# Optimization experiments

Hardware: AMD Instinct MI355X
Metric: run time of the kernel (lower is better)

The kernel has to match this reference:

```python
import jax, jax.numpy as jnp
import numpy as np

B = 131072
_CNOT_PERM = np.array([0, 1, 3, 2])  # |c t>: 10<->11 swap


def _apply_1q(psi, mats, wire):
    # psi: [B,2,2,2,2] complex, mats: [B,2,2] complex, per-sample single-qubit gate on `wire`
    psi = jnp.moveaxis(psi, wire + 1, -1)
    sh = psi.shape
    psi = psi.reshape(sh[0], -1, 2)
    psi = jnp.einsum('bij,bkj->bki', mats, psi)
    return jnp.moveaxis(psi.reshape(sh), -1, wire + 1)


def _cnot_adj(psi, w):
    # CNOT with control=w, target=w+1 (adjacent wires)
    psi = jnp.moveaxis(psi, (w + 1, w + 2), (-2, -1))
    sh = psi.shape
    psi = psi.reshape(sh[:-2] + (4,))[..., _CNOT_PERM].reshape(sh)
    return jnp.moveaxis(psi, (-2, -1), (w + 1, w + 2))


def _circuit(enc):
    # enc: [B,4] rotation angles; returns [B,4] PauliZ expectations
    b = enc.shape[0]
    half = 0.5 * enc
    c = jnp.cos(half).astype(jnp.complex64)
    s = jnp.sin(half).astype(jnp.complex64)
    z = jnp.zeros_like(c)
    ph = jnp.exp(-1j * half.astype(jnp.complex64))
    ry = jnp.stack([jnp.stack([c, -s], -1), jnp.stack([s, c], -1)], -2)   # [B,4,2,2]
    rz = jnp.stack([jnp.stack([ph, z], -1), jnp.stack([z, jnp.conj(ph)], -1)], -2)
    rx = jnp.stack([jnp.stack([c, -1j * s], -1), jnp.stack([-1j * s, c], -1)], -2)
    psi = jnp.zeros((b, 2, 2, 2, 2), jnp.complex64).at[:, 0, 0, 0, 0].set(1.0)
    for w in range(4):
        psi = _apply_1q(psi, ry[:, w], w)
    for w in range(4):
        psi = _apply_1q(psi, rz[:, w], w)
    for w in range(3):
        psi = _cnot_adj(psi, w)
    for w in range(4):
        psi = _apply_1q(psi, rx[:, w], w)
    probs = psi.real ** 2 + psi.imag ** 2  # [B,2,2,2,2]
    expz = []
    for w in range(4):
        p = jnp.moveaxis(probs, w + 1, 1).reshape(b, 2, -1).sum(-1)
        expz.append(p[:, 0] - p[:, 1])
    return jnp.stack(expz, -1)  # [B,4]


def setup_inputs() -> dict:
    key = jax.random.key(0)
    ks = jax.random.split(key, 9)
    f32 = jnp.float32
    return {
        'x': jax.random.normal(ks[0], (B, 1, 24, 24), f32),
        'W_enc': jax.random.normal(ks[1], (4, 16), f32) * 0.25,
        'b_enc': jax.random.normal(ks[2], (4,), f32) * 0.25,
        'W1': jax.random.normal(ks[3], (32, 4), f32) * 0.5,
        'b1': jax.random.normal(ks[4], (32,), f32) * 0.5,
        'W2': jax.random.normal(ks[5], (4, 32), f32) * 0.17,
        'b2': jax.random.normal(ks[6], (4,), f32) * 0.17,
        'gamma': jnp.ones((4,), f32),
        'beta': jnp.zeros((4,), f32),
    }


def reference(x, W_enc, b_enc, W1, b1, W2, b2, gamma, beta):
    bsz = x.shape[0]
    # avg_pool2d(x, 6): 24x24 -> 4x4, then flatten to 16
    pooled = x.reshape(bsz, 1, 4, 6, 4, 6).mean((3, 5)).reshape(bsz, 16)
    encoded = pooled @ W_enc.T + b_enc            # [B,4]
    out_q = _circuit(encoded)                      # [B,4]
    h = jax.nn.relu(out_q @ W1.T + b1)             # [B,32]
    out = h @ W2.T + b2                            # [B,num_classes]
    # BatchNorm1d in training mode (biased batch variance, eps=1e-5)
    mean = out.mean(0)
    var = ((out - mean) ** 2).mean(0)
    return gamma * (out - mean) / jnp.sqrt(var + 1e-5) + beta
```

## Files before the change

### kernel.cpp

```cpp
#include <hip/hip_runtime.h>

#define BATCH   131072
#define NBLK    512

__global__ __launch_bounds__(256) void qnat_main(
    const float* __restrict__ x,
    const float* __restrict__ Wenc, const float* __restrict__ benc,
    const float* __restrict__ W1,   const float* __restrict__ b1,
    const float* __restrict__ W2,   const float* __restrict__ b2,
    float* __restrict__ out_pre, float* __restrict__ partials)
{
    __shared__ float sW[360];
    const int t = threadIdx.x;
    if (t < 64)  sW[t]       = Wenc[t];
    if (t < 4)   sW[64 + t]  = benc[t];
    if (t < 128) sW[68 + t]  = W1[t];
    if (t < 32)  sW[196 + t] = b1[t];
    if (t < 128) sW[228 + t] = W2[t];
    if (t < 4)   sW[356 + t] = b2[t];
    __syncthreads();

    const int s = blockIdx.x * 256 + t;
    const float4* xp = reinterpret_cast<const float4*>(x + (size_t)s * 576);

    float pooled[16];
    #pragma unroll
    for (int pr = 0; pr < 4; ++pr) {
        float a0 = 0.f, a1 = 0.f, a2 = 0.f, a3 = 0.f;
        #pragma unroll
        for (int rr = 0; rr < 6; ++rr) {
            const float4* row = xp + (pr * 6 + rr) * 6;
            float4 va = row[0], vb = row[1], vc = row[2];
            float4 vd = row[3], ve = row[4], vf = row[5];
            a0 += va.x + va.y + va.z + va.w + vb.x + vb.y;
            a1 += vb.z + vb.w + vc.x + vc.y + vc.z + vc.w;
            a2 += vd.x + vd.y + vd.z + vd.w + ve.x + ve.y;
            a3 += ve.z + ve.w + vf.x + vf.y + vf.z + vf.w;
        }
        pooled[pr * 4 + 0] = a0 * (1.f / 36.f);
        pooled[pr * 4 + 1] = a1 * (1.f / 36.f);
        pooled[pr * 4 + 2] = a2 * (1.f / 36.f);
        pooled[pr * 4 + 3] = a3 * (1.f / 36.f);
    }

    float ch[4], sh[4];
    #pragma unroll
    for (int j = 0; j < 4; ++j) {
        float e = sW[64 + j];
        #pragma unroll
        for (int k = 0; k < 16; ++k) e = fmaf(pooled[k], sW[j * 16 + k], e);
        const float h = 0.5f * e;
        ch[j] = cosf(h);
        sh[j] = sinf(h);
    }

    float re[16], im[16];
    #pragma unroll
    for (int i = 0; i < 16; ++i) { re[i] = 0.f; im[i] = 0.f; }
    re[0] = 1.f;

    #pragma unroll
    for (int w = 0; w < 4; ++w) {
        const int bit = 8 >> w;
        #pragma unroll
        for (int i = 0; i < 16; ++i) if (!(i & bit)) {
            const int j = i | bit;
            const float r0 = re[i], m0 = im[i], r1 = re[j], m1 = im[j];
            re[i] = ch[w] * r0 - sh[w] * r1;  im[i] = ch[w] * m0 - sh[w] * m1;
            re[j] = sh[w] * r0 + ch[w] * r1;  im[j] = sh[w] * m0 + ch[w] * m1;
        }
    }
    #pragma unroll
    for (int w = 0; w < 4; ++w) {
        const int bit = 8 >> w;
        #pragma unroll
        for (int i = 0; i < 16; ++i) {
            const float sg = (i & bit) ? 1.f : -1.f;
            const float r = re[i], m = im[i];
            re[i] = ch[w] * r - sg * sh[w] * m;
            im[i] = ch[w] * m + sg * sh[w] * r;
        }
    }
    #define SWAP_AMP(a, b) { float tr = re[a]; re[a] = re[b]; re[b] = tr; \
                             float ti = im[a]; im[a] = im[b]; im[b] = ti; }
    SWAP_AMP(8, 12)  SWAP_AMP(9, 13)  SWAP_AMP(10, 14) SWAP_AMP(11, 15)
    SWAP_AMP(4, 6)   SWAP_AMP(5, 7)   SWAP_AMP(12, 14) SWAP_AMP(13, 15)
    SWAP_AMP(2, 3)   SWAP_AMP(6, 7)   SWAP_AMP(10, 11) SWAP_AMP(14, 15)
    #undef SWAP_AMP

    #pragma unroll
    for (int w = 0; w < 4; ++w) {
        const int bit = 8 >> w;
        #pragma unroll
        for (int i = 0; i < 16; ++i) if (!(i & bit)) {
            const int j = i | bit;
            const float r0 = re[i], m0 = im[i], r1 = re[j], m1 = im[j];
            re[i] = ch[w] * r0 + sh[w] * m1;  im[i] = ch[w] * m0 - sh[w] * r1;
            re[j] = sh[w] * m0 + ch[w] * r1;  im[j] = ch[w] * m1 - sh[w] * r0;
        }
    }

    float ez[4];
    #pragma unroll
    for (int w = 0; w < 4; ++w) {
        const int bit = 8 >> w;
        float acc = 0.f;
        #pragma unroll
        for (int i = 0; i < 16; ++i) {
            const float p = re[i] * re[i] + im[i] * im[i];
            acc += (i & bit) ? -p : p;
        }
        ez[w] = acc;
    }

    float o0 = sW[356], o1 = sW[357], o2 = sW[358], o3 = sW[359];
    #pragma unroll
    for (int i = 0; i < 32; ++i) {
        float h = sW[196 + i];
        #pragma unroll
        for (int j = 0; j < 4; ++j) h = fmaf(ez[j], sW[68 + i * 4 + j], h);
        h = fmaxf(h, 0.f);
        o0 = fmaf(h, sW[228 +  0 + i], o0);
        o1 = fmaf(h, sW[228 + 32 + i], o1);
        o2 = fmaf(h, sW[228 + 64 + i], o2);
        o3 = fmaf(h, sW[228 + 96 + i], o3);
    }

    reinterpret_cast<float4*>(out_pre)[s] = make_float4(o0, o1, o2, o3);

    float v[8] = { o0, o1, o2, o3, o0 * o0, o1 * o1, o2 * o2, o3 * o3 };
    #pragma unroll
    for (int off = 32; off; off >>= 1) {
        #pragma unroll
        for (int k = 0; k < 8; ++k) v[k] += __shfl_down(v[k], off);
    }
    __shared__ float red[4][8];
    const int wave = t >> 6, lane = t & 63;
    if (lane == 0) {
        #pragma unroll
        for (int k = 0; k < 8; ++k) red[wave][k] = v[k];
    }
    __syncthreads();
    if (t < 8) {
        partials[blockIdx.x * 8 + t] = red[0][t] + red[1][t] + red[2][t] + red[3][t];
    }
}

__global__ __launch_bounds__(512) void qnat_reduce(
    const float* __restrict__ partials, const float* __restrict__ gamma,
    const float* __restrict__ beta, float* __restrict__ ss)
{
    const int t = threadIdx.x;
    const float4* p4 = reinterpret_cast<const float4*>(partials);
    const float4 a = p4[t * 2], b = p4[t * 2 + 1];
    float v[8] = { a.x, a.y, a.z, a.w, b.x, b.y, b.z, b.w };
    #pragma unroll
    for (int off = 32; off; off >>= 1) {
        #pragma unroll
        for (int k = 0; k < 8; ++k) v[k] += __shfl_down(v[k], off);
    }
    __shared__ float red[8][8];
    const int wave = t >> 6, lane = t & 63;
    if (lane == 0) {
        #pragma unroll
        for (int k = 0; k < 8; ++k) red[wave][k] = v[k];
    }
    __syncthreads();
    if (t < 4) {
        float sum = 0.f, sumsq = 0.f;
        #pragma unroll
        for (int w = 0; w < 8; ++w) { sum += red[w][t]; sumsq += red[w][4 + t]; }
        const float invB  = 1.f / (float)BATCH;
        const float mean  = sum * invB;
        const float var   = sumsq * invB - mean * mean;
        const float scale = gamma[t] / sqrtf(var + 1e-5f);
        ss[t]     = scale;
        ss[4 + t] = beta[t] - mean * scale;
    }
}

__global__ __launch_bounds__(256) void qnat_bn(
    float* __restrict__ io, const float* __restrict__ ss)
{
    __shared__ float s8[8];
    if (threadIdx.x < 8) s8[threadIdx.x] = ss[threadIdx.x];
    __syncthreads();
    const int idx = blockIdx.x * 256 + threadIdx.x;
    float4* p = reinterpret_cast<float4*>(io);
    float4 v = p[idx];
    v.x = fmaf(v.x, s8[0], s8[4]);
    v.y = fmaf(v.y, s8[1], s8[5]);
    v.z = fmaf(v.z, s8[2], s8[6]);
    v.w = fmaf(v.w, s8[3], s8[7]);
    p[idx] = v;
}

extern "C" void kernel_launch(void* const* d_in, const int* in_sizes, int n_in,
                              void* d_out, int out_size, void* d_ws, size_t ws_size,
                              hipStream_t stream)
{
    const float* x     = (const float*)d_in[0];
    const float* Wenc  = (const float*)d_in[1];
    const float* benc  = (const float*)d_in[2];
    const float* W1    = (const float*)d_in[3];
    const float* b1    = (const float*)d_in[4];
    const float* W2    = (const float*)d_in[5];
    const float* b2    = (const float*)d_in[6];
    const float* gamma = (const float*)d_in[7];
    const float* beta  = (const float*)d_in[8];

    float* out      = (float*)d_out;
    float* partials = (float*)d_ws;
    float* ss       = partials + NBLK * 8;

    qnat_main<<<NBLK, 256, 0, stream>>>(x, Wenc, benc, W1, b1, W2, b2, out, partials);
    qnat_reduce<<<1, 512, 0, stream>>>(partials, gamma, beta, ss);
    qnat_bn<<<NBLK, 256, 0, stream>>>(out, ss);
}
```

Measured before the change: 71.71 us.

## Fuse main, reduce and batchnorm kernels via cooperative grid sync

Merges the three kernels into one cooperative kernel. After each block writes its partial sums, a grid-wide sync lets every block reduce all partials redundantly and apply batchnorm directly to its in-register outputs. This removes two kernel launches and the write-then-reread of the pre-normalized output. In exchange it adds a grid barrier, redundant per-block reduction of 4096 partials, and depends on all 512 blocks being co-resident.

New measurement: 152.8 us. 2.13x slower.

```diff
diff --git a/kernel.cpp b/kernel.cpp
--- a/kernel.cpp
+++ b/kernel.cpp
@@ -1,16 +1,21 @@
 #include <hip/hip_runtime.h>
+#include <hip/hip_cooperative_groups.h>
+
+namespace cg = cooperative_groups;
 
 #define BATCH   131072
 #define NBLK    512
 
-__global__ __launch_bounds__(256) void qnat_main(
+__global__ __launch_bounds__(256, 2) void qnat_fused(
     const float* __restrict__ x,
     const float* __restrict__ Wenc, const float* __restrict__ benc,
     const float* __restrict__ W1,   const float* __restrict__ b1,
     const float* __restrict__ W2,   const float* __restrict__ b2,
-    float* __restrict__ out_pre, float* __restrict__ partials)
+    const float* __restrict__ gamma, const float* __restrict__ beta,
+    float* __restrict__ out, float* __restrict__ partials)
 {
     __shared__ float sW[360];
+    __shared__ float red[4][8];
     const int t = threadIdx.x;
     if (t < 64)  sW[t]       = Wenc[t];
     if (t < 4)   sW[64 + t]  = benc[t];
@@ -126,73 +131,61 @@
         o3 = fmaf(h, sW[228 + 96 + i], o3);
     }
 
-    reinterpret_cast<float4*>(out_pre)[s] = make_float4(o0, o1, o2, o3);
-
-    float v[8] = { o0, o1, o2, o3, o0 * o0, o1 * o1, o2 * o2, o3 * o3 };
-    #pragma unroll
-    for (int off = 32; off; off >>= 1) {
-        #pragma unroll
-        for (int k = 0; k < 8; ++k) v[k] += __shfl_down(v[k], off);
-    }
-    __shared__ float red[4][8];
-    const int wave = t >> 6, lane = t & 63;
-    if (lane == 0) {
-        #pragma unroll
-        for (int k = 0; k < 8; ++k) red[wave][k] = v[k];
-    }
-    __syncthreads();
-    if (t < 8) {
-        partials[blockIdx.x * 8 + t] = red[0][t] + red[1][t] + red[2][t] + red[3][t];
-    }
-}
-
-__global__ __launch_bounds__(512) void qnat_reduce(
-    const float* __restrict__ partials, const float* __restrict__ gamma,
-    const float* __restrict__ beta, float* __restrict__ ss)
-{
-    const int t = threadIdx.x;
-    const float4* p4 = reinterpret_cast<const float4*>(partials);
-    const float4 a = p4[t * 2], b = p4[t * 2 + 1];
-    float v[8] = { a.x, a.y, a.z, a.w, b.x, b.y, b.z, b.w };
-    #pragma unroll
-    for (int off = 32; off; off >>= 1) {
-        #pragma unroll
-        for (int k = 0; k < 8; ++k) v[k] += __shfl_down(v[k], off);
-    }
-    __shared__ float red[8][8];
-    const int wave = t >> 6, lane = t & 63;
-    if (lane == 0) {
-        #pragma unroll
-        for (int k = 0; k < 8; ++k) red[wave][k] = v[k];
-    }
-    __syncthreads();
-    if (t < 4) {
-        float sum = 0.f, sumsq = 0.f;
-        #pragma unroll
-        for (int w = 0; w < 8; ++w) { sum += red[w][t]; sumsq += red[w][4 + t]; }
+    {
+        float v[8] = { o0, o1, o2, o3, o0 * o0, o1 * o1, o2 * o2, o3 * o3 };
+        #pragma unroll
+        for (int off = 32; off; off >>= 1) {
+            #pragma unroll
+            for (int k = 0; k < 8; ++k) v[k] += __shfl_down(v[k], off);
+        }
+        const int wave = t >> 6, lane = t & 63;
+        if (lane == 0) {
+            #pragma unroll
+            for (int k = 0; k < 8; ++k) red[wave][k] = v[k];
+        }
+        __syncthreads();
+        if (t < 8) {
+            partials[blockIdx.x * 8 + t] = red[0][t] + red[1][t] + red[2][t] + red[3][t];
+        }
+    }
+
+    cg::this_grid().sync();
+
+    {
+        const float4* p4 = reinterpret_cast<const float4*>(partials);
+        const float4 a0 = p4[t * 4 + 0], a1 = p4[t * 4 + 1];
+        const float4 a2 = p4[t * 4 + 2], a3 = p4[t * 4 + 3];
+        float v[8] = { a0.x + a2.x, a0.y + a2.y, a0.z + a2.z, a0.w + a2.w,
+                       a1.x + a3.x, a1.y + a3.y, a1.z + a3.z, a1.w + a3.w };
+        #pragma unroll
+        for (int off = 32; off; off >>= 1) {
+            #pragma unroll
+            for (int k = 0; k < 8; ++k) v[k] += __shfl_down(v[k], off);
+        }
+        const int wave = t >> 6, lane = t & 63;
+        __syncthreads();
+        if (lane == 0) {
+            #pragma unroll
+            for (int k = 0; k < 8; ++k) red[wave][k] = v[k];
+        }
+        __syncthreads();
+    }
+
+    float sc[4], sf[4];
+    #pragma unroll
+    for (int j = 0; j < 4; ++j) {
+        const float sum   = red[0][j] + red[1][j] + red[2][j] + red[3][j];
+        const float sumsq = red[0][4 + j] + red[1][4 + j] + red[2][4 + j] + red[3][4 + j];
         const float invB  = 1.f / (float)BATCH;
         const float mean  = sum * invB;
         const float var   = sumsq * invB - mean * mean;
-        const float scale = gamma[t] / sqrtf(var + 1e-5f);
-        ss[t]     = scale;
-        ss[4 + t] = beta[t] - mean * scale;
-    }
-}
-
-__global__ __launch_bounds__(256) void qnat_bn(
-    float* __restrict__ io, const float* __restrict__ ss)
-{
-    __shared__ float s8[8];
-    if (threadIdx.x < 8) s8[threadIdx.x] = ss[threadIdx.x];
-    __syncthreads();
-    const int idx = blockIdx.x * 256 + threadIdx.x;
-    float4* p = reinterpret_cast<float4*>(io);
-    float4 v = p[idx];
-    v.x = fmaf(v.x, s8[0], s8[4]);
-    v.y = fmaf(v.y, s8[1], s8[5]);
-    v.z = fmaf(v.z, s8[2], s8[6]);
-    v.w = fmaf(v.w, s8[3], s8[7]);
-    p[idx] = v;
+        sc[j] = gamma[j] / sqrtf(var + 1e-5f);
+        sf[j] = beta[j] - mean * sc[j];
+    }
+
+    reinterpret_cast<float4*>(out)[s] = make_float4(
+        fmaf(o0, sc[0], sf[0]), fmaf(o1, sc[1], sf[1]),
+        fmaf(o2, sc[2], sf[2]), fmaf(o3, sc[3], sf[3]));
 }
 
 extern "C" void kernel_launch(void* const* d_in, const int* in_sizes, int n_in,
@@ -211,9 +204,10 @@
 
     float* out      = (float*)d_out;
     float* partials = (float*)d_ws;
-    float* ss       = partials + NBLK * 8;
-
-    qnat_main<<<NBLK, 256, 0, stream>>>(x, Wenc, benc, W1, b1, W2, b2, out, partials);
-    qnat_reduce<<<1, 512, 0, stream>>>(partials, gamma, beta, ss);
-    qnat_bn<<<NBLK, 256, 0, stream>>>(out, ss);
+
+    void* args[] = { (void*)&x, (void*)&Wenc, (void*)&benc, (void*)&W1, (void*)&b1,
+                     (void*)&W2, (void*)&b2, (void*)&gamma, (void*)&beta,
+                     (void*)&out, (void*)&partials };
+    hipLaunchCooperativeKernel((void*)qnat_fused, dim3(NBLK), dim3(256),
+                               args, 0, stream);
 }
```

## Split each sample across four threads for pooling and encoder dot products

Applied to the files above, without the earlier changes.

Each sample is now handled by a quad of four threads: each thread pools one 6-row band and computes a partial encoder dot product, combined with xor shuffles. The quantum simulation and MLP are recomputed redundantly in all four threads, and each thread writes one output feature. This raises the main grid from 512 to 2048 blocks to expose more parallelism for the memory-bound pooling, and the reduce kernel is changed to consume four times as many partials. The cost is four-fold redundant compute on the circuit and MLP and extra shuffles.

New measurement: 99.34 us. 38.5% more time.

```diff
diff --git a/kernel.cpp b/kernel.cpp
--- a/kernel.cpp
+++ b/kernel.cpp
@@ -1,9 +1,10 @@
 #include <hip/hip_runtime.h>
 
-#define BATCH   131072
-#define NBLK    512
-
-__global__ __launch_bounds__(256) void qnat_main(
+#define BATCH      131072
+#define NBLK_MAIN  2048
+#define NBLK_BN    512
+
+__global__ __launch_bounds__(256, 8) void qnat_main(
     const float* __restrict__ x,
     const float* __restrict__ Wenc, const float* __restrict__ benc,
     const float* __restrict__ W1,   const float* __restrict__ b1,
@@ -11,6 +12,7 @@
     float* __restrict__ out_pre, float* __restrict__ partials)
 {
     __shared__ float sW[360];
+    __shared__ float redS[4][4], redQ[4][4];
     const int t = threadIdx.x;
     if (t < 64)  sW[t]       = Wenc[t];
     if (t < 4)   sW[64 + t]  = benc[t];
@@ -20,36 +22,34 @@
     if (t < 4)   sW[356 + t] = b2[t];
     __syncthreads();
 
-    const int s = blockIdx.x * 256 + t;
-    const float4* xp = reinterpret_cast<const float4*>(x + (size_t)s * 576);
-
-    float pooled[16];
-    #pragma unroll
-    for (int pr = 0; pr < 4; ++pr) {
-        float a0 = 0.f, a1 = 0.f, a2 = 0.f, a3 = 0.f;
-        #pragma unroll
-        for (int rr = 0; rr < 6; ++rr) {
-            const float4* row = xp + (pr * 6 + rr) * 6;
-            float4 va = row[0], vb = row[1], vc = row[2];
-            float4 vd = row[3], ve = row[4], vf = row[5];
-            a0 += va.x + va.y + va.z + va.w + vb.x + vb.y;
-            a1 += vb.z + vb.w + vc.x + vc.y + vc.z + vc.w;
-            a2 += vd.x + vd.y + vd.z + vd.w + ve.x + ve.y;
-            a3 += ve.z + ve.w + vf.x + vf.y + vf.z + vf.w;
-        }
-        pooled[pr * 4 + 0] = a0 * (1.f / 36.f);
-        pooled[pr * 4 + 1] = a1 * (1.f / 36.f);
-        pooled[pr * 4 + 2] = a2 * (1.f / 36.f);
-        pooled[pr * 4 + 3] = a3 * (1.f / 36.f);
-    }
+    const int gid = blockIdx.x * 64 + (t >> 2);
+    const int k   = t & 3;
+    const float4* xp = reinterpret_cast<const float4*>(
+        x + (size_t)gid * 576 + k * 144);
+
+    float a0 = 0.f, a1 = 0.f, a2 = 0.f, a3 = 0.f;
+    #pragma unroll
+    for (int rr = 0; rr < 6; ++rr) {
+        const float4* row = xp + rr * 6;
+        float4 va = row[0], vb = row[1], vc = row[2];
+        float4 vd = row[3], ve = row[4], vf = row[5];
+        a0 += va.x + va.y + va.z + va.w + vb.x + vb.y;
+        a1 += vb.z + vb.w + vc.x + vc.y + vc.z + vc.w;
+        a2 += vd.x + vd.y + vd.z + vd.w + ve.x + ve.y;
+        a3 += ve.z + ve.w + vf.x + vf.y + vf.z + vf.w;
+    }
+    const float pk[4] = { a0 * (1.f / 36.f), a1 * (1.f / 36.f),
+                          a2 * (1.f / 36.f), a3 * (1.f / 36.f) };
 
     float ch[4], sh[4];
     #pragma unroll
     for (int j = 0; j < 4; ++j) {
-        float e = sW[64 + j];
-        #pragma unroll
-        for (int k = 0; k < 16; ++k) e = fmaf(pooled[k], sW[j * 16 + k], e);
-        const float h = 0.5f * e;
+        float e = 0.f;
+        #pragma unroll
+        for (int c = 0; c < 4; ++c) e = fmaf(pk[c], sW[j * 16 + k * 4 + c], e);
+        e += __shfl_xor(e, 1);
+        e += __shfl_xor(e, 2);
+        const float h = 0.5f * (e + sW[64 + j]);
         ch[j] = cosf(h);
         sh[j] = sinf(h);
     }
@@ -126,23 +126,24 @@
         o3 = fmaf(h, sW[228 + 96 + i], o3);
     }
 
-    reinterpret_cast<float4*>(out_pre)[s] = make_float4(o0, o1, o2, o3);
-
-    float v[8] = { o0, o1, o2, o3, o0 * o0, o1 * o1, o2 * o2, o3 * o3 };
-    #pragma unroll
-    for (int off = 32; off; off >>= 1) {
-        #pragma unroll
-        for (int k = 0; k < 8; ++k) v[k] += __shfl_down(v[k], off);
-    }
-    __shared__ float red[4][8];
+    const float ov = (k == 0) ? o0 : (k == 1) ? o1 : (k == 2) ? o2 : o3;
+    out_pre[(size_t)blockIdx.x * 256 + t] = ov;
+
+    float vs = ov, vq = ov * ov;
+    #pragma unroll
+    for (int off = 32; off >= 4; off >>= 1) {
+        vs += __shfl_down(vs, off);
+        vq += __shfl_down(vq, off);
+    }
     const int wave = t >> 6, lane = t & 63;
-    if (lane == 0) {
-        #pragma unroll
-        for (int k = 0; k < 8; ++k) red[wave][k] = v[k];
-    }
+    if (lane < 4) { redS[wave][lane] = vs; redQ[wave][lane] = vq; }
     __syncthreads();
     if (t < 8) {
-        partials[blockIdx.x * 8 + t] = red[0][t] + red[1][t] + red[2][t] + red[3][t];
+        const int f = t & 3;
+        const float r = (t < 4)
+            ? (redS[0][f] + redS[1][f] + redS[2][f] + redS[3][f])
+            : (redQ[0][f] + redQ[1][f] + redQ[2][f] + redQ[3][f]);
+        partials[blockIdx.x * 8 + t] = r;
     }
 }
 
@@ -152,18 +153,23 @@
 {
     const int t = threadIdx.x;
     const float4* p4 = reinterpret_cast<const float4*>(partials);
-    const float4 a = p4[t * 2], b = p4[t * 2 + 1];
-    float v[8] = { a.x, a.y, a.z, a.w, b.x, b.y, b.z, b.w };
+    float v[8] = { 0.f, 0.f, 0.f, 0.f, 0.f, 0.f, 0.f, 0.f };
+    #pragma unroll
+    for (int r = 0; r < 4; ++r) {
+        const float4 a = p4[t * 8 + r * 2], b = p4[t * 8 + r * 2 + 1];
+        v[0] += a.x; v[1] += a.y; v[2] += a.z; v[3] += a.w;
+        v[4] += b.x; v[5] += b.y; v[6] += b.z; v[7] += b.w;
+    }
     #pragma unroll
     for (int off = 32; off; off >>= 1) {
         #pragma unroll
-        for (int k = 0; k < 8; ++k) v[k] += __shfl_down(v[k], off);
+        for (int kk = 0; kk < 8; ++kk) v[kk] += __shfl_down(v[kk], off);
     }
     __shared__ float red[8][8];
     const int wave = t >> 6, lane = t & 63;
     if (lane == 0) {
         #pragma unroll
-        for (int k = 0; k < 8; ++k) red[wave][k] = v[k];
+        for (int kk = 0; kk < 8; ++kk) red[wave][kk] = v[kk];
     }
     __syncthreads();
     if (t < 4) {
@@ -211,9 +217,10 @@
 
     float* out      = (float*)d_out;
     float* partials = (float*)d_ws;
-    float* ss       = partials + NBLK * 8;
-
-    qnat_main<<<NBLK, 256, 0, stream>>>(x, Wenc, benc, W1, b1, W2, b2, out, partials);
+    float* ss       = partials + NBLK_MAIN * 8;
+
+    qnat_main<<<NBLK_MAIN, 256, 0, stream>>>(x, Wenc, benc, W1, b1, W2, b2,
+                                             out, partials);
     qnat_reduce<<<1, 512, 0, stream>>>(partials, gamma, beta, ss);
-    qnat_bn<<<NBLK, 256, 0, stream>>>(out, ss);
-}
+    qnat_bn<<<NBLK_BN, 256, 0, stream>>>(out, ss);
+}
```

## Coalesce pooling input loads via per-wave LDS staging and transpose

Applied to the files above, without the earlier changes.

Replaces per-thread strided float4 reads of each 576-float sample with wave-cooperative coalesced loads of four samples at a time, staged in shared memory. Each lane then computes one pooled cell, and the pooled values are transposed back to per-sample ownership through a padded LDS buffer. This targets uncoalesced global access in the memory-bound pooling stage, at the cost of about 54 KB of LDS per block, extra LDS traffic, and reduced occupancy.

Result: faster. 59.77 us (-16.6%).

```diff
diff --git a/kernel.cpp b/kernel.cpp
--- a/kernel.cpp
+++ b/kernel.cpp
@@ -1,9 +1,10 @@
 #include <hip/hip_runtime.h>
 
-#define BATCH   131072
-#define NBLK    512
-
-__global__ __launch_bounds__(256) void qnat_main(
+#define BATCH      131072
+#define NBLK_MAIN  512
+#define NBLK_BN    512
+
+__global__ __launch_bounds__(256, 2) void qnat_main(
     const float* __restrict__ x,
     const float* __restrict__ Wenc, const float* __restrict__ benc,
     const float* __restrict__ W1,   const float* __restrict__ b1,
@@ -11,6 +12,10 @@
     float* __restrict__ out_pre, float* __restrict__ partials)
 {
     __shared__ float sW[360];
+    __shared__ __align__(16) float stage[4][2320];
+    __shared__ float pbuf[4][1088];
+    __shared__ float redS[4][8];
+
     const int t = threadIdx.x;
     if (t < 64)  sW[t]       = Wenc[t];
     if (t < 4)   sW[64 + t]  = benc[t];
@@ -20,28 +25,51 @@
     if (t < 4)   sW[356 + t] = b2[t];
     __syncthreads();
 
-    const int s = blockIdx.x * 256 + t;
-    const float4* xp = reinterpret_cast<const float4*>(x + (size_t)s * 576);
-
+    const int wave = t >> 6, lane = t & 63;
+    const int sampleBase = blockIdx.x * 256 + wave * 64;
+    float* st = stage[wave];
+    float* pb = pbuf[wave];
+
+    const int s_loc = lane >> 4;
+    const int slot  = lane & 15;
+    const int spr   = slot >> 2, spc = slot & 3;
+    const int rdOff = s_loc * 580 + spr * 144 + spc * 6;
+
+    const float4* xg = reinterpret_cast<const float4*>(x);
+    const unsigned gbase = (unsigned)sampleBase * 144u;
+
+    float pv[16];
+    #pragma unroll
+    for (int c = 0; c < 16; ++c) {
+        float4 v[9];
+        #pragma unroll
+        for (int i = 0; i < 9; ++i)
+            v[i] = xg[gbase + (unsigned)c * 576u + (unsigned)i * 64u + (unsigned)lane];
+        #pragma unroll
+        for (int i = 0; i < 9; ++i) {
+            const int g = i * 64 + lane;
+            const int s = g / 144;
+            const int q = g - s * 144;
+            *reinterpret_cast<float4*>(&st[s * 580 + q * 4]) = v[i];
+        }
+        float acc = 0.f;
+        #pragma unroll
+        for (int r = 0; r < 6; ++r) {
+            const float2 a  = *reinterpret_cast<const float2*>(&st[rdOff + r * 24 + 0]);
+            const float2 bb = *reinterpret_cast<const float2*>(&st[rdOff + r * 24 + 2]);
+            const float2 cc = *reinterpret_cast<const float2*>(&st[rdOff + r * 24 + 4]);
+            acc += a.x + a.y + bb.x + bb.y + cc.x + cc.y;
+        }
+        pv[c] = acc * (1.f / 36.f);
+    }
+
+    #pragma unroll
+    for (int c = 0; c < 16; ++c)
+        pb[(c * 4 + s_loc) * 17 + slot] = pv[c];
     float pooled[16];
     #pragma unroll
-    for (int pr = 0; pr < 4; ++pr) {
-        float a0 = 0.f, a1 = 0.f, a2 = 0.f, a3 = 0.f;
-        #pragma unroll
-        for (int rr = 0; rr < 6; ++rr) {
-            const float4* row = xp + (pr * 6 + rr) * 6;
-            float4 va = row[0], vb = row[1], vc = row[2];
-            float4 vd = row[3], ve = row[4], vf = row[5];
-            a0 += va.x + va.y + va.z + va.w + vb.x + vb.y;
-            a1 += vb.z + vb.w + vc.x + vc.y + vc.z + vc.w;
-            a2 += vd.x + vd.y + vd.z + vd.w + ve.x + ve.y;
-            a3 += ve.z + ve.w + vf.x + vf.y + vf.z + vf.w;
-        }
-        pooled[pr * 4 + 0] = a0 * (1.f / 36.f);
-        pooled[pr * 4 + 1] = a1 * (1.f / 36.f);
-        pooled[pr * 4 + 2] = a2 * (1.f / 36.f);
-        pooled[pr * 4 + 3] = a3 * (1.f / 36.f);
-    }
+    for (int q = 0; q < 16; ++q)
+        pooled[q] = pb[lane * 17 + q];
 
     float ch[4], sh[4];
     #pragma unroll
@@ -64,10 +92,10 @@
         const int bit = 8 >> w;
         #pragma unroll
         for (int i = 0; i < 16; ++i) if (!(i & bit)) {
-            const int j = i | bit;
-            const float r0 = re[i], m0 = im[i], r1 = re[j], m1 = im[j];
-            re[i] = ch[w] * r0 - sh[w] * r1;  im[i] = ch[w] * m0 - sh[w] * m1;
-            re[j] = sh[w] * r0 + ch[w] * r1;  im[j] = sh[w] * m0 + ch[w] * m1;
+            const int jj = i | bit;
+            const float r0 = re[i], m0 = im[i], r1 = re[jj], m1 = im[jj];
+            re[i]  = ch[w] * r0 - sh[w] * r1;  im[i]  = ch[w] * m0 - sh[w] * m1;
+            re[jj] = sh[w] * r0 + ch[w] * r1;  im[jj] = sh[w] * m0 + ch[w] * m1;
         }
     }
     #pragma unroll
@@ -93,10 +121,10 @@
         const int bit = 8 >> w;
         #pragma unroll
         for (int i = 0; i < 16; ++i) if (!(i & bit)) {
-            const int j = i | bit;
-            const float r0 = re[i], m0 = im[i], r1 = re[j], m1 = im[j];
-            re[i] = ch[w] * r0 + sh[w] * m1;  im[i] = ch[w] * m0 - sh[w] * r1;
-            re[j] = sh[w] * m0 + ch[w] * r1;  im[j] = ch[w] * m1 - sh[w] * r0;
+            const int jj = i | bit;
+            const float r0 = re[i], m0 = im[i], r1 = re[jj], m1 = im[jj];
+            re[i]  = ch[w] * r0 + sh[w] * m1;  im[i]  = ch[w] * m0 - sh[w] * r1;
+            re[jj] = sh[w] * m0 + ch[w] * r1;  im[jj] = ch[w] * m1 - sh[w] * r0;
         }
     }
 
@@ -126,23 +154,25 @@
         o3 = fmaf(h, sW[228 + 96 + i], o3);
     }
 
-    reinterpret_cast<float4*>(out_pre)[s] = make_float4(o0, o1, o2, o3);
-
-    float v[8] = { o0, o1, o2, o3, o0 * o0, o1 * o1, o2 * o2, o3 * o3 };
-    #pragma unroll
-    for (int off = 32; off; off >>= 1) {
-        #pragma unroll
-        for (int k = 0; k < 8; ++k) v[k] += __shfl_down(v[k], off);
-    }
-    __shared__ float red[4][8];
-    const int wave = t >> 6, lane = t & 63;
-    if (lane == 0) {
-        #pragma unroll
-        for (int k = 0; k < 8; ++k) red[wave][k] = v[k];
-    }
-    __syncthreads();
-    if (t < 8) {
-        partials[blockIdx.x * 8 + t] = red[0][t] + red[1][t] + red[2][t] + red[3][t];
+    reinterpret_cast<float4*>(out_pre)[blockIdx.x * 256 + t] =
+        make_float4(o0, o1, o2, o3);
+
+    {
+        float v8[8] = { o0, o1, o2, o3, o0 * o0, o1 * o1, o2 * o2, o3 * o3 };
+        #pragma unroll
+        for (int off = 32; off; off >>= 1) {
+            #pragma unroll
+            for (int k = 0; k < 8; ++k) v8[k] += __shfl_down(v8[k], off);
+        }
+        if (lane == 0) {
+            #pragma unroll
+            for (int k = 0; k < 8; ++k) redS[wave][k] = v8[k];
+        }
+        __syncthreads();
+        if (t < 8) {
+            partials[blockIdx.x * 8 + t] =
+                redS[0][t] + redS[1][t] + redS[2][t] + redS[3][t];
+        }
     }
 }
 
@@ -211,9 +241,10 @@
 
     float* out      = (float*)d_out;
     float* partials = (float*)d_ws;
-    float* ss       = partials + NBLK * 8;
-
-    qnat_main<<<NBLK, 256, 0, stream>>>(x, Wenc, benc, W1, b1, W2, b2, out, partials);
+    float* ss       = partials + NBLK_MAIN * 8;
+
+    qnat_main<<<NBLK_MAIN, 256, 0, stream>>>(x, Wenc, benc, W1, b1, W2, b2,
+                                             out, partials);
     qnat_reduce<<<1, 512, 0, stream>>>(partials, gamma, beta, ss);
-    qnat_bn<<<NBLK, 256, 0, stream>>>(out, ss);
-}
+    qnat_bn<<<NBLK_BN, 256, 0, stream>>>(out, ss);
+}
```
